# Optimization experiments

Hardware: AMD Instinct MI355X
Metric: run time of the kernel (lower is better)

The kernel has to match this reference:

```python
import jax, jax.numpy as jnp
import numpy as np

V, H_BASE, D, L, K = 32000, 4096, 512, 2, 4
B = 64

def setup_inputs() -> dict:
    key = jax.random.key(0)
    ks = jax.random.split(key, 12)
    s = 0.02
    return {
        "hidden_state": jax.random.normal(ks[0], (B, H_BASE), jnp.float32),
        "in_proj_w": jax.random.normal(ks[1], (D, H_BASE), jnp.float32) * s,
        "in_proj_b": jnp.zeros((D,), jnp.float32),
        "w_ih0": jax.random.normal(ks[2], (3 * D, D), jnp.float32) * s,
        "w_hh0": jax.random.normal(ks[3], (3 * D, D), jnp.float32) * s,
        "b_ih0": jax.random.normal(ks[4], (3 * D,), jnp.float32) * s,
        "b_hh0": jax.random.normal(ks[5], (3 * D,), jnp.float32) * s,
        "w_ih1": jax.random.normal(ks[6], (3 * D, D), jnp.float32) * s,
        "w_hh1": jax.random.normal(ks[7], (3 * D, D), jnp.float32) * s,
        "b_ih1": jax.random.normal(ks[8], (3 * D,), jnp.float32) * s,
        "b_hh1": jax.random.normal(ks[9], (3 * D,), jnp.float32) * s,
        "embed": jax.random.normal(ks[10], (V, D), jnp.float32) * s,
        "out_w": jax.random.normal(ks[11], (V, D), jnp.float32) * s,
    }

def _gru_cell(x, h, w_ih, w_hh, b_ih, b_hh):
    # PyTorch GRU gate order: r, z, n
    gi = x @ w_ih.T + b_ih  # [B, 3D]
    gh = h @ w_hh.T + b_hh
    ir, iz, inn = jnp.split(gi, 3, axis=-1)
    hr, hz, hn = jnp.split(gh, 3, axis=-1)
    r = jax.nn.sigmoid(ir + hr)
    z = jax.nn.sigmoid(iz + hz)
    n = jnp.tanh(inn + r * hn)
    return (1.0 - z) * n + z * h

def reference(hidden_state, in_proj_w, in_proj_b, w_ih0, w_hh0, b_ih0, b_hh0,
              w_ih1, w_hh1, b_ih1, b_hh1, embed, out_w):
    b = hidden_state.shape[0]
    h0 = hidden_state @ in_proj_w.T + in_proj_b  # [B, D]
    h_l0 = h0
    h_l1 = h0
    x = jnp.zeros((b, in_proj_w.shape[0]), hidden_state.dtype)
    all_logits = []
    for _ in range(K):
        h_l0 = _gru_cell(x, h_l0, w_ih0, w_hh0, b_ih0, b_hh0)
        h_l1 = _gru_cell(h_l0, h_l1, w_ih1, w_hh1, b_ih1, b_hh1)
        logits = h_l1 @ out_w.T  # [B, V]
        all_logits.append(logits)
        x = embed[jnp.argmax(logits, axis=-1)]  # greedy next-token embed
    return jnp.stack(all_logits, axis=1)  # [B, K, V]
```

## Files before the change

kernel.cpp:

```cpp
#include <hip/hip_runtime.h>
#include <math.h>


typedef __attribute__((ext_vector_type(8))) short short8;
typedef __attribute__((ext_vector_type(4))) float f32x4;

__device__ __forceinline__ unsigned short f2bf_rne(float x) {
    unsigned u = __float_as_uint(x);
    unsigned r = (u + 0x7fffu + ((u >> 16) & 1u)) >> 16;
    return (unsigned short)r;
}
__device__ __forceinline__ void split2(float x, unsigned short& hi, unsigned short& lo) {
    unsigned u = __float_as_uint(x);
    hi = (unsigned short)(u >> 16);
    float r = x - __uint_as_float(u & 0xffff0000u);
    lo = f2bf_rne(r);
}

__device__ __forceinline__ void store_plane(unsigned short* hiP, unsigned short* loP,
                                            int m, int d, float v) {
    int s = d >> 6, cl = (d >> 3) & 7, e = d & 7;
    int off = m * 512 + s * 64 + ((cl ^ (m & 7)) * 8) + e;
    unsigned short hi, lo; split2(v, hi, lo);
    hiP[off] = hi; loP[off] = lo;
}

__device__ __forceinline__ void gload16(const void* g, void* lds) {
    __builtin_amdgcn_global_load_lds(
        (const __attribute__((address_space(1))) unsigned int*)g,
        (__attribute__((address_space(3))) unsigned int*)lds, 16, 0, 0);
}

__device__ __forceinline__ void split_w_body(
    const float* __restrict__ W, unsigned short* __restrict__ H,
    unsigned short* __restrict__ L, size_t g, int kclog)
{
    int n  = (int)(g >> kclog);
    int c8 = (int)g & ((1 << kclog) - 1);
    const float* src = W + g * 8;
    float4 v0 = *(const float4*)src;
    float4 v1 = *(const float4*)(src + 4);
    unsigned short h[8], l[8];
    split2(v0.x,h[0],l[0]); split2(v0.y,h[1],l[1]); split2(v0.z,h[2],l[2]); split2(v0.w,h[3],l[3]);
    split2(v1.x,h[4],l[4]); split2(v1.y,h[5],l[5]); split2(v1.z,h[6],l[6]); split2(v1.w,h[7],l[7]);
    uint4 ph = make_uint4((unsigned)h[0]|((unsigned)h[1]<<16), (unsigned)h[2]|((unsigned)h[3]<<16),
                          (unsigned)h[4]|((unsigned)h[5]<<16), (unsigned)h[6]|((unsigned)h[7]<<16));
    uint4 pl = make_uint4((unsigned)l[0]|((unsigned)l[1]<<16), (unsigned)l[2]|((unsigned)l[3]<<16),
                          (unsigned)l[4]|((unsigned)l[5]<<16), (unsigned)l[6]|((unsigned)l[7]<<16));
    int nt = n >> 7, row = n & 127;
    int ksi = c8 >> 3;
    int slot = (c8 & 7) ^ (row & 7);
    int tpr = 1 << (kclog - 3);
    size_t off = ((size_t)(nt * tpr + ksi) * 128 + row) * 64 + slot * 8;
    *(uint4*)(H + off) = ph;
    *(uint4*)(L + off) = pl;
}

__global__ __launch_bounds__(256) void k_split_W(
    const float* __restrict__ W, unsigned short* __restrict__ H,
    unsigned short* __restrict__ L, int kclog)
{
    size_t g = (size_t)blockIdx.x * 256 + threadIdx.x;
    split_w_body(W, H, L, g, kclog);
}

__global__ __launch_bounds__(256) void k_split_gw(
    const float* __restrict__ w0, const float* __restrict__ w1,
    const float* __restrict__ w2, const float* __restrict__ w3,
    unsigned short* __restrict__ H, unsigned short* __restrict__ L)
{
    int mat = blockIdx.y;
    const float* W = mat == 0 ? w0 : mat == 1 ? w1 : mat == 2 ? w2 : w3;
    size_t g = (size_t)blockIdx.x * 256 + threadIdx.x;
    split_w_body(W, H + (size_t)mat * 786432, L + (size_t)mat * 786432, g, 6);
}

__global__ __launch_bounds__(256) void k_split_A(
    const float* __restrict__ hidden, char* __restrict__ hidH, char* __restrict__ hidL)
{
    int g = blockIdx.x * 256 + threadIdx.x;
    int m = g >> 9;
    int cc = g & 511;
    int s = cc >> 3, cl = cc & 7;
    const float* src = hidden + m * 4096 + cc * 8;
    float4 v0 = *(const float4*)src;
    float4 v1 = *(const float4*)(src + 4);
    unsigned short h[8], l[8];
    split2(v0.x,h[0],l[0]); split2(v0.y,h[1],l[1]); split2(v0.z,h[2],l[2]); split2(v0.w,h[3],l[3]);
    split2(v1.x,h[4],l[4]); split2(v1.y,h[5],l[5]); split2(v1.z,h[6],l[6]); split2(v1.w,h[7],l[7]);
    uint4 ph = make_uint4((unsigned)h[0]|((unsigned)h[1]<<16), (unsigned)h[2]|((unsigned)h[3]<<16),
                          (unsigned)h[4]|((unsigned)h[5]<<16), (unsigned)h[6]|((unsigned)h[7]<<16));
    uint4 pl = make_uint4((unsigned)l[0]|((unsigned)l[1]<<16), (unsigned)l[2]|((unsigned)l[3]<<16),
                          (unsigned)l[4]|((unsigned)l[5]<<16), (unsigned)l[6]|((unsigned)l[7]<<16));
    int off = m * 8192 + s * 128 + ((cl ^ (m & 7)) * 16);
    *(uint4*)(hidH + off) = ph;
    *(uint4*)(hidL + off) = pl;
}

__device__ __forceinline__ void mfma_core(
    const unsigned short* __restrict__ AsH0, const unsigned short* __restrict__ AsL0,
    const unsigned short* __restrict__ BsH0, const unsigned short* __restrict__ BsL0,
    int wv, int lr, int lh, f32x4* acc)
{
#pragma unroll
    for (int kk2 = 0; kk2 < 2; ++kk2) {
        int aoff = lr * 64 + (((kk2 * 4 + lh) ^ (lr & 7)) * 8);
        short8 ah[4], al[4];
#pragma unroll
        for (int mt = 0; mt < 4; ++mt) {
            ah[mt] = *(const short8*)(AsH0 + mt * 1024 + aoff);
            al[mt] = *(const short8*)(AsL0 + mt * 1024 + aoff);
        }
        int brow = wv * 16 + lr;
        int boff = brow * 64 + (((kk2 * 4 + lh) ^ (brow & 7)) * 8);
        short8 bh = *(const short8*)(BsH0 + boff);
        short8 bl = *(const short8*)(BsL0 + boff);
#pragma unroll
        for (int mt = 0; mt < 4; ++mt) {
            acc[mt] = __builtin_amdgcn_mfma_f32_16x16x32_bf16(ah[mt], bh, acc[mt], 0, 0, 0);
            acc[mt] = __builtin_amdgcn_mfma_f32_16x16x32_bf16(ah[mt], bl, acc[mt], 0, 0, 0);
            acc[mt] = __builtin_amdgcn_mfma_f32_16x16x32_bf16(al[mt], bh, acc[mt], 0, 0, 0);
        }
    }
}

__device__ __forceinline__ void epilogue_write(
    float* __restrict__ C, int ldc, int n0, int wv, int lr, int lh, const f32x4* acc)
{
#pragma unroll
    for (int mt = 0; mt < 4; ++mt)
#pragma unroll
        for (int i = 0; i < 4; ++i) {
            int mm = mt * 16 + lh * 4 + i;
            C[mm * ldc + n0 + wv * 16 + lr] = acc[mt][i];
        }
}

__device__ __forceinline__ void mfma_gemm4(
    const char* __restrict__ AH, const char* __restrict__ AL, int AstrideB, int akk0,
    const unsigned short* __restrict__ BH, const unsigned short* __restrict__ BL,
    size_t btileU, int nk,
    float* __restrict__ C, int ldc, int n0,
    unsigned short (*AsH)[4096], unsigned short (*AsL)[4096],
    unsigned short (*BsH)[4096], unsigned short (*BsL)[4096])
{
    const int tid  = threadIdx.x;
    const int wv   = tid >> 6;
    const int lane = tid & 63;
    const int lr   = lane & 15;
    const int lh   = lane >> 4;
    const int ar1  = wv * 16 + (lane >> 3);
    const int acp  = lane & 7;

    f32x4 acc[4];
#pragma unroll
    for (int i = 0; i < 4; ++i) acc[i] = (f32x4){0.f, 0.f, 0.f, 0.f};

    auto stage = [&](int t, int p) {
        const int kaB = (akk0 + t * 64) * 2;
        gload16(AH + ar1 * AstrideB + kaB + acp * 16,       (char*)AsH[p] + wv * 2048);
        gload16(AH + (ar1 + 8) * AstrideB + kaB + acp * 16, (char*)AsH[p] + wv * 2048 + 1024);
        gload16(AL + ar1 * AstrideB + kaB + acp * 16,       (char*)AsL[p] + wv * 2048);
        gload16(AL + (ar1 + 8) * AstrideB + kaB + acp * 16, (char*)AsL[p] + wv * 2048 + 1024);
        const char* bH = (const char*)BH + (btileU + (size_t)t * 8192) * 2;
        const char* bL = (const char*)BL + (btileU + (size_t)t * 8192) * 2;
        gload16(bH + wv * 2048 +        lane * 16, (char*)BsH[p] + wv * 2048);
        gload16(bH + wv * 2048 + 1024 + lane * 16, (char*)BsH[p] + wv * 2048 + 1024);
        gload16(bL + wv * 2048 +        lane * 16, (char*)BsL[p] + wv * 2048);
        gload16(bL + wv * 2048 + 1024 + lane * 16, (char*)BsL[p] + wv * 2048 + 1024);
    };

    stage(0, 0);
    __syncthreads();

    for (int t = 0; t < nk; ++t) {
        const int p = t & 1;
        if (t + 1 < nk) stage(t + 1, p ^ 1);
        mfma_core(AsH[p], AsL[p], BsH[p], BsL[p], wv, lr, lh, acc);
        __syncthreads();
    }

    epilogue_write(C, ldc, n0, wv, lr, lh, acc);
}

#define DECLARE_LDS4() \
    __shared__ alignas(16) unsigned short AsH[2][4096]; \
    __shared__ alignas(16) unsigned short AsL[2][4096]; \
    __shared__ alignas(16) unsigned short BsH[2][4096]; \
    __shared__ alignas(16) unsigned short BsL[2][4096];

__global__ __launch_bounds__(256) void k_inproj(
    const char* __restrict__ hidH, const char* __restrict__ hidL,
    const unsigned short* __restrict__ WH, const unsigned short* __restrict__ WL,
    float* __restrict__ part)
{
    DECLARE_LDS4();
    int nt2 = blockIdx.x & 7;
    int ks  = blockIdx.x >> 3;
    size_t btile = (size_t)((nt2 >> 1) * 64 + ks * 4) * 8192 + (size_t)(nt2 & 1) * 4096;
    mfma_gemm4(hidH, hidL, 8192, ks * 256,
               WH, WL, btile, 4,
               part + ks * 32768, 512, nt2 * 64,
               AsH, AsL, BsH, BsL);
}

__global__ __launch_bounds__(256) void k_reduce_inproj(
    const float* __restrict__ part, const float* __restrict__ bias,
    float* __restrict__ hA, float* __restrict__ hB,
    unsigned short* hAH, unsigned short* hAL,
    unsigned short* hBH, unsigned short* hBL,
    unsigned short* xH,  unsigned short* xL)
{
    int i = blockIdx.x * 256 + threadIdx.x;
    int b = i >> 9;
    int d = i & 511;
    float s = bias[d];
#pragma unroll
    for (int ks = 0; ks < 16; ++ks) s += part[ks * 32768 + i];
    hA[i] = s;
    hB[i] = s;
    store_plane(hAH, hAL, b, d, s);
    store_plane(hBH, hBL, b, d, s);
    store_plane(xH,  xL,  b, d, 0.f);
}

__global__ __launch_bounds__(256) void k_gates(
    const char* __restrict__ xH, const char* __restrict__ xL,
    const char* __restrict__ hH, const char* __restrict__ hL,
    const unsigned short* __restrict__ gwH, const unsigned short* __restrict__ gwL,
    int layer, float* __restrict__ gip, float* __restrict__ ghp)
{
    DECLARE_LDS4();
    int bx  = blockIdx.x;
    int nt2 = bx % 24;
    int ks  = (bx / 24) & 3;
    int mat = bx / 96;
    const char* AH = mat ? hH : xH;
    const char* AL = mat ? hL : xL;
    float* C = (mat ? ghp : gip) + ks * 98304;
    size_t btile = ((size_t)(layer * 2 + mat) * 96 + (nt2 >> 1) * 8 + ks * 2) * 8192
                 + (size_t)(nt2 & 1) * 4096;
    mfma_gemm4(AH, AL, 1024, ks * 128,
               gwH, gwL, btile, 2,
               C, 1536, nt2 * 64,
               AsH, AsL, BsH, BsL);
}

__global__ __launch_bounds__(256) void k_combine(
    const float* __restrict__ gip, const float* __restrict__ ghp,
    const float* __restrict__ b_ih, const float* __restrict__ b_hh,
    float* __restrict__ h, unsigned short* hH, unsigned short* hL)
{
    int i = blockIdx.x * 256 + threadIdx.x;
    int b = i >> 9;
    int d = i & 511;
    int base = b * 1536 + d;
    float ir = b_ih[d], iz = b_ih[d + 512], inn = b_ih[d + 1024];
    float hr = b_hh[d], hz = b_hh[d + 512], hn = b_hh[d + 1024];
#pragma unroll
    for (int ks = 0; ks < 4; ++ks) {
        const float* gi = gip + ks * 98304 + base;
        const float* gh = ghp + ks * 98304 + base;
        ir  += gi[0];    iz += gi[512];  inn += gi[1024];
        hr  += gh[0];    hz += gh[512];  hn  += gh[1024];
    }
    float r = 1.f / (1.f + expf(-(ir + hr)));
    float z = 1.f / (1.f + expf(-(iz + hz)));
    float n = tanhf(inn + r * hn);
    float hv = (1.f - z) * n + z * h[i];
    h[i] = hv;
    store_plane(hH, hL, b, d, hv);
}

__global__ __launch_bounds__(256) void k_logits(
    const char* __restrict__ hBH, const char* __restrict__ hBL,
    const float* __restrict__ out_w,
    float* __restrict__ out, int step,
    float* __restrict__ pval, int* __restrict__ pidx)
{
    __shared__ alignas(16) unsigned short AsH[2][4096];
    __shared__ alignas(16) unsigned short AsL[2][4096];
    __shared__ alignas(16) unsigned short BsH[2][4096];
    __shared__ alignas(16) unsigned short BsL[2][4096];

    const int tid  = threadIdx.x;
    const int wv   = tid >> 6;
    const int lane = tid & 63;
    const int lr   = lane & 15;
    const int lh   = lane >> 4;
    const int bx   = blockIdx.x;
    const int n0   = bx * 64;

    const int ar1 = wv * 16 + (lane >> 3);
    const int acp = lane & 7;
    auto stageA = [&](int kaB, int p) {
        gload16(hBH + ar1 * 1024 + kaB + acp * 16,       (char*)AsH[p] + wv * 2048);
        gload16(hBH + (ar1 + 8) * 1024 + kaB + acp * 16, (char*)AsH[p] + wv * 2048 + 1024);
        gload16(hBL + ar1 * 1024 + kaB + acp * 16,       (char*)AsL[p] + wv * 2048);
        gload16(hBL + (ar1 + 8) * 1024 + kaB + acp * 16, (char*)AsL[p] + wv * 2048 + 1024);
    };

    const int bn = tid >> 2, bq = tid & 3;
    const float* Wb = out_w + (size_t)(n0 + bn) * 512 + bq * 16;
    const int wo0 = bn * 64 + (((2 * bq)     ^ (bn & 7)) * 8);
    const int wo1 = bn * 64 + (((2 * bq + 1) ^ (bn & 7)) * 8);

    float4 r0, r1, r2, r3;
    auto loadB = [&](int t) {
        const float* s = Wb + t * 64;
        r0 = *(const float4*)s;       r1 = *(const float4*)(s + 4);
        r2 = *(const float4*)(s + 8); r3 = *(const float4*)(s + 12);
    };
    auto writeB = [&](int p) {
        unsigned short h[16], l[16];
        split2(r0.x,h[0],l[0]);   split2(r0.y,h[1],l[1]);   split2(r0.z,h[2],l[2]);   split2(r0.w,h[3],l[3]);
        split2(r1.x,h[4],l[4]);   split2(r1.y,h[5],l[5]);   split2(r1.z,h[6],l[6]);   split2(r1.w,h[7],l[7]);
        split2(r2.x,h[8],l[8]);   split2(r2.y,h[9],l[9]);   split2(r2.z,h[10],l[10]); split2(r2.w,h[11],l[11]);
        split2(r3.x,h[12],l[12]); split2(r3.y,h[13],l[13]); split2(r3.z,h[14],l[14]); split2(r3.w,h[15],l[15]);
        *(uint4*)(BsH[p] + wo0) = make_uint4(
            (unsigned)h[0]|((unsigned)h[1]<<16),  (unsigned)h[2]|((unsigned)h[3]<<16),
            (unsigned)h[4]|((unsigned)h[5]<<16),  (unsigned)h[6]|((unsigned)h[7]<<16));
        *(uint4*)(BsH[p] + wo1) = make_uint4(
            (unsigned)h[8]|((unsigned)h[9]<<16),  (unsigned)h[10]|((unsigned)h[11]<<16),
            (unsigned)h[12]|((unsigned)h[13]<<16),(unsigned)h[14]|((unsigned)h[15]<<16));
        *(uint4*)(BsL[p] + wo0) = make_uint4(
            (unsigned)l[0]|((unsigned)l[1]<<16),  (unsigned)l[2]|((unsigned)l[3]<<16),
            (unsigned)l[4]|((unsigned)l[5]<<16),  (unsigned)l[6]|((unsigned)l[7]<<16));
        *(uint4*)(BsL[p] + wo1) = make_uint4(
            (unsigned)l[8]|((unsigned)l[9]<<16),  (unsigned)l[10]|((unsigned)l[11]<<16),
            (unsigned)l[12]|((unsigned)l[13]<<16),(unsigned)l[14]|((unsigned)l[15]<<16));
    };

    f32x4 acc[4];
#pragma unroll
    for (int i = 0; i < 4; ++i) acc[i] = (f32x4){0.f, 0.f, 0.f, 0.f};

    loadB(0);
    stageA(0, 0);
    writeB(0);
    __syncthreads();
#pragma unroll
    for (int t = 0; t < 8; ++t) {
        const int p = t & 1;
        if (t < 7) { loadB(t + 1); stageA((t + 1) * 128, p ^ 1); }
        mfma_core(AsH[p], AsL[p], BsH[p], BsL[p], wv, lr, lh, acc);
        if (t < 7) writeB(p ^ 1);
        __syncthreads();
    }

    epilogue_write(out + step * 32000, 128000, n0, wv, lr, lh, acc);

    float* sv = (float*)&AsH[0][0];
    int*   sc = (int*)&AsL[0][0];
#pragma unroll
    for (int mt = 0; mt < 4; ++mt)
#pragma unroll
        for (int i = 0; i < 4; ++i) {
            float v = acc[mt][i];
            int   c = n0 + wv * 16 + lr;
#pragma unroll
            for (int msk = 1; msk < 16; msk <<= 1) {
                float ov = __shfl_xor(v, msk, 64);
                int   oc = __shfl_xor(c, msk, 64);
                if (ov > v || (ov == v && oc < c)) { v = ov; c = oc; }
            }
            if (lr == 0) {
                int row = mt * 16 + lh * 4 + i;
                sv[wv * 64 + row] = v;
                sc[wv * 64 + row] = c;
            }
        }
    __syncthreads();
    if (tid < 64) {
        float v = sv[tid]; int c = sc[tid];
#pragma unroll
        for (int w = 1; w < 4; ++w) {
            float ov = sv[w * 64 + tid]; int oc = sc[w * 64 + tid];
            if (ov > v || (ov == v && oc < c)) { v = ov; c = oc; }
        }
        pval[bx * 64 + tid] = v;
        pidx[bx * 64 + tid] = c;
    }
}

__global__ __launch_bounds__(256) void k_reduce_embed(
    const float* __restrict__ pval, const int* __restrict__ pidx,
    const float* __restrict__ embed, unsigned short* xH, unsigned short* xL)
{
    __shared__ float sv[256];
    __shared__ int   sc[256];
    const int b = blockIdx.x;
    const int tid = threadIdx.x;
    float v = pval[tid * 64 + b];
    int   c = pidx[tid * 64 + b];
    if (tid + 256 < 500) {
        float ov = pval[(tid + 256) * 64 + b];
        int   oc = pidx[(tid + 256) * 64 + b];
        if (ov > v || (ov == v && oc < c)) { v = ov; c = oc; }
    }
    sv[tid] = v; sc[tid] = c;
    __syncthreads();
    for (int s = 128; s > 0; s >>= 1) {
        if (tid < s) {
            float ov = sv[tid + s]; int oc = sc[tid + s];
            if (ov > sv[tid] || (ov == sv[tid] && oc < sc[tid])) { sv[tid] = ov; sc[tid] = oc; }
        }
        __syncthreads();
    }
    int tok = sc[0];
    for (int j = tid; j < 512; j += 256)
        store_plane(xH, xL, b, j, embed[(size_t)tok * 512 + j]);
}

extern "C" void kernel_launch(void* const* d_in, const int* in_sizes, int n_in,
                              void* d_out, int out_size, void* d_ws, size_t ws_size,
                              hipStream_t stream)
{
    const float* hidden = (const float*)d_in[0];
    const float* in_w   = (const float*)d_in[1];
    const float* in_b   = (const float*)d_in[2];
    const float* w_ih0  = (const float*)d_in[3];
    const float* w_hh0  = (const float*)d_in[4];
    const float* b_ih0  = (const float*)d_in[5];
    const float* b_hh0  = (const float*)d_in[6];
    const float* w_ih1  = (const float*)d_in[7];
    const float* w_hh1  = (const float*)d_in[8];
    const float* b_ih1  = (const float*)d_in[9];
    const float* b_hh1  = (const float*)d_in[10];
    const float* embed  = (const float*)d_in[11];
    const float* out_w  = (const float*)d_in[12];
    float* out = (float*)d_out;
    char*  ws  = (char*)d_ws;

    float* hA  = (float*)(ws + 0);
    float* hB  = (float*)(ws + 131072);
    unsigned short* xH  = (unsigned short*)(ws + 262144);
    unsigned short* xL  = (unsigned short*)(ws + 327680);
    unsigned short* hAH = (unsigned short*)(ws + 393216);
    unsigned short* hAL = (unsigned short*)(ws + 458752);
    unsigned short* hBH = (unsigned short*)(ws + 524288);
    unsigned short* hBL = (unsigned short*)(ws + 589824);
    char* hidH = ws + 655360;
    char* hidL = ws + 1179648;
    float* gip = (float*)(ws + 1703936);
    float* ghp = (float*)(ws + 3276800);
    float* pval = (float*)(ws + 4849664);
    int*   pidx = (int*)  (ws + 4980736);
    float* ipart = (float*)(ws + 5111808);
    unsigned short* gwH = (unsigned short*)(ws + 7208960);
    unsigned short* gwL = (unsigned short*)(ws + 13500416);
    unsigned short* inH = (unsigned short*)(ws + 19791872);
    unsigned short* inL = (unsigned short*)(ws + 23986176);

    k_split_A<<<128, 256, 0, stream>>>(hidden, hidH, hidL);
    k_split_gw<<<dim3(384, 4), 256, 0, stream>>>(w_ih0, w_hh0, w_ih1, w_hh1, gwH, gwL);
    k_split_W<<<1024, 256, 0, stream>>>(in_w, inH, inL, 9);
    k_inproj<<<128, 256, 0, stream>>>(hidH, hidL, inH, inL, ipart);
    k_reduce_inproj<<<128, 256, 0, stream>>>(ipart, in_b, hA, hB,
                                             hAH, hAL, hBH, hBL, xH, xL);

    for (int step = 0; step < 4; ++step) {
        k_gates<<<192, 256, 0, stream>>>((char*)xH, (char*)xL, (char*)hAH, (char*)hAL,
                                         gwH, gwL, 0, gip, ghp);
        k_combine<<<128, 256, 0, stream>>>(gip, ghp, b_ih0, b_hh0, hA, hAH, hAL);
        k_gates<<<192, 256, 0, stream>>>((char*)hAH, (char*)hAL, (char*)hBH, (char*)hBL,
                                         gwH, gwL, 1, gip, ghp);
        k_combine<<<128, 256, 0, stream>>>(gip, ghp, b_ih1, b_hh1, hB, hBH, hBL);
        k_logits<<<500, 256, 0, stream>>>((char*)hBH, (char*)hBL, out_w,
                                          out, step, pval, pidx);
        k_reduce_embed<<<64, 256, 0, stream>>>(pval, pidx, embed, xH, xL);
    }
}
```

Measured before the change: 353.2 us.

## Fuse argmax reduction and embedding gather into layer-0 gate GEMM

Removes the separate argmax-reduce/embed kernel. Each layer-0 input-gate block now redoes the final argmax over transposed partial results and splits the gathered embedding rows into its own LDS A tile. At step 0 it just writes zeros, since x is zero. This saves one launch per step and the round trip of x through global memory, at the cost of every one of the 96 input-gate blocks repeating the 64x500 argmax reduction.

```diff
diff --git a/kernel.cpp b/kernel.cpp
--- a/kernel.cpp
+++ b/kernel.cpp
@@ -208,8 +208,7 @@
     const float* __restrict__ part, const float* __restrict__ bias,
     float* __restrict__ hA, float* __restrict__ hB,
     unsigned short* hAH, unsigned short* hAL,
-    unsigned short* hBH, unsigned short* hBL,
-    unsigned short* xH,  unsigned short* xL)
+    unsigned short* hBH, unsigned short* hBL)
 {
     int i = blockIdx.x * 256 + threadIdx.x;
     int b = i >> 9;
@@ -221,7 +220,104 @@
     hB[i] = s;
     store_plane(hAH, hAL, b, d, s);
     store_plane(hBH, hBL, b, d, s);
-    store_plane(xH,  xL,  b, d, 0.f);
+}
+
+__global__ __launch_bounds__(256) void k_gates_l0(
+    int step,
+    const float* __restrict__ pvT, const int* __restrict__ piT,
+    const float* __restrict__ embed,
+    const char* __restrict__ hAH, const char* __restrict__ hAL,
+    const unsigned short* __restrict__ gwH, const unsigned short* __restrict__ gwL,
+    float* __restrict__ gip, float* __restrict__ ghp)
+{
+    DECLARE_LDS4();
+    __shared__ int stok[64];
+    const int bx = blockIdx.x, tid = threadIdx.x;
+    const int nt2 = bx % 24, ks = (bx / 24) & 3, mat = bx / 96;
+
+    if (mat) {
+        size_t btile = ((size_t)96 + (nt2 >> 1) * 8 + ks * 2) * 8192
+                     + (size_t)(nt2 & 1) * 4096;
+        mfma_gemm4(hAH, hAL, 1024, ks * 128, gwH, gwL, btile, 2,
+                   ghp + ks * 98304, 1536, nt2 * 64, AsH, AsL, BsH, BsL);
+        return;
+    }
+
+    float* C = gip + ks * 98304;
+    if (step == 0) {
+        float4 z = make_float4(0.f, 0.f, 0.f, 0.f);
+        for (int q = tid; q < 1024; q += 256) {
+            int r2 = q >> 4, cq = q & 15;
+            *(float4*)(C + r2 * 1536 + nt2 * 64 + cq * 4) = z;
+        }
+        return;
+    }
+
+    const int wv = tid >> 6, lane = tid & 63, lr = lane & 15, lh = lane >> 4;
+    const size_t btileU = ((size_t)((nt2 >> 1) * 8 + ks * 2)) * 8192
+                        + (size_t)(nt2 & 1) * 4096;
+    auto stageB = [&](int t, int p) {
+        const char* bH = (const char*)gwH + (btileU + (size_t)t * 8192) * 2;
+        const char* bL = (const char*)gwL + (btileU + (size_t)t * 8192) * 2;
+        gload16(bH + wv * 2048 +        lane * 16, (char*)BsH[p] + wv * 2048);
+        gload16(bH + wv * 2048 + 1024 + lane * 16, (char*)BsH[p] + wv * 2048 + 1024);
+        gload16(bL + wv * 2048 +        lane * 16, (char*)BsL[p] + wv * 2048);
+        gload16(bL + wv * 2048 + 1024 + lane * 16, (char*)BsL[p] + wv * 2048 + 1024);
+    };
+
+    stageB(0, 0);
+
+    {
+        int r = tid >> 2, j0 = tid & 3;
+        float v = -3.4e38f; int c = 0x7fffffff;
+        for (int j = j0; j < 500; j += 4) {
+            float ov = pvT[r * 512 + j]; int oc = piT[r * 512 + j];
+            if (ov > v || (ov == v && oc < c)) { v = ov; c = oc; }
+        }
+#pragma unroll
+        for (int msk = 1; msk < 4; msk <<= 1) {
+            float ov = __shfl_xor(v, msk, 64);
+            int   oc = __shfl_xor(c, msk, 64);
+            if (ov > v || (ov == v && oc < c)) { v = ov; c = oc; }
+        }
+        if (j0 == 0) stok[r] = c;
+    }
+    __syncthreads();
+
+    {
+        int mm = tid >> 2, cl0 = (tid & 3) * 2;
+        int tok = stok[mm];
+        int obase = (mm >> 4) * 1024 + (mm & 15) * 64;
+#pragma unroll
+        for (int t2 = 0; t2 < 2; ++t2) {
+#pragma unroll
+            for (int u = 0; u < 2; ++u) {
+                int cl = cl0 + u;
+                const float* src = embed + (size_t)tok * 512 + ks * 128 + t2 * 64 + cl * 8;
+                float4 v0 = *(const float4*)src;
+                float4 v1 = *(const float4*)(src + 4);
+                unsigned short h[8], l[8];
+                split2(v0.x,h[0],l[0]); split2(v0.y,h[1],l[1]); split2(v0.z,h[2],l[2]); split2(v0.w,h[3],l[3]);
+                split2(v1.x,h[4],l[4]); split2(v1.y,h[5],l[5]); split2(v1.z,h[6],l[6]); split2(v1.w,h[7],l[7]);
+                uint4 ph = make_uint4((unsigned)h[0]|((unsigned)h[1]<<16), (unsigned)h[2]|((unsigned)h[3]<<16),
+                                      (unsigned)h[4]|((unsigned)h[5]<<16), (unsigned)h[6]|((unsigned)h[7]<<16));
+                uint4 pl = make_uint4((unsigned)l[0]|((unsigned)l[1]<<16), (unsigned)l[2]|((unsigned)l[3]<<16),
+                                      (unsigned)l[4]|((unsigned)l[5]<<16), (unsigned)l[6]|((unsigned)l[7]<<16));
+                int off = obase + ((cl ^ (mm & 7)) * 8);
+                *(uint4*)(AsH[t2] + off) = ph;
+                *(uint4*)(AsL[t2] + off) = pl;
+            }
+        }
+    }
+    stageB(1, 1);
+    __syncthreads();
+
+    f32x4 acc[4];
+#pragma unroll
+    for (int i = 0; i < 4; ++i) acc[i] = (f32x4){0.f, 0.f, 0.f, 0.f};
+    mfma_core(AsH[0], AsL[0], BsH[0], BsL[0], wv, lr, lh, acc);
+    mfma_core(AsH[1], AsL[1], BsH[1], BsL[1], wv, lr, lh, acc);
+    epilogue_write(C, 1536, nt2 * 64, wv, lr, lh, acc);
 }
 
 __global__ __launch_bounds__(256) void k_gates(
@@ -276,7 +372,7 @@
     const char* __restrict__ hBH, const char* __restrict__ hBL,
     const float* __restrict__ out_w,
     float* __restrict__ out, int step,
-    float* __restrict__ pval, int* __restrict__ pidx)
+    float* __restrict__ pvT, int* __restrict__ piT)
 {
     __shared__ alignas(16) unsigned short AsH[2][4096];
     __shared__ alignas(16) unsigned short AsL[2][4096];
@@ -378,38 +474,9 @@
             float ov = sv[w * 64 + tid]; int oc = sc[w * 64 + tid];
             if (ov > v || (ov == v && oc < c)) { v = ov; c = oc; }
         }
-        pval[bx * 64 + tid] = v;
-        pidx[bx * 64 + tid] = c;
-    }
-}
-
-__global__ __launch_bounds__(256) void k_reduce_embed(
-    const float* __restrict__ pval, const int* __restrict__ pidx,
-    const float* __restrict__ embed, unsigned short* xH, unsigned short* xL)
-{
-    __shared__ float sv[256];
-    __shared__ int   sc[256];
-    const int b = blockIdx.x;
-    const int tid = threadIdx.x;
-    float v = pval[tid * 64 + b];
-    int   c = pidx[tid * 64 + b];
-    if (tid + 256 < 500) {
-        float ov = pval[(tid + 256) * 64 + b];
-        int   oc = pidx[(tid + 256) * 64 + b];
-        if (ov > v || (ov == v && oc < c)) { v = ov; c = oc; }
-    }
-    sv[tid] = v; sc[tid] = c;
-    __syncthreads();
-    for (int s = 128; s > 0; s >>= 1) {
-        if (tid < s) {
-            float ov = sv[tid + s]; int oc = sc[tid + s];
-            if (ov > sv[tid] || (ov == sv[tid] && oc < sc[tid])) { sv[tid] = ov; sc[tid] = oc; }
-        }
-        __syncthreads();
-    }
-    int tok = sc[0];
-    for (int j = tid; j < 512; j += 256)
-        store_plane(xH, xL, b, j, embed[(size_t)tok * 512 + j]);
+        pvT[tid * 512 + bx] = v;
+        piT[tid * 512 + bx] = c;
+    }
 }
 
 extern "C" void kernel_launch(void* const* d_in, const int* in_sizes, int n_in,
@@ -434,8 +501,6 @@
 
     float* hA  = (float*)(ws + 0);
     float* hB  = (float*)(ws + 131072);
-    unsigned short* xH  = (unsigned short*)(ws + 262144);
-    unsigned short* xL  = (unsigned short*)(ws + 327680);
     unsigned short* hAH = (unsigned short*)(ws + 393216);
     unsigned short* hAL = (unsigned short*)(ws + 458752);
     unsigned short* hBH = (unsigned short*)(ws + 524288);
@@ -444,8 +509,8 @@
     char* hidL = ws + 1179648;
     float* gip = (float*)(ws + 1703936);
     float* ghp = (float*)(ws + 3276800);
-    float* pval = (float*)(ws + 4849664);
-    int*   pidx = (int*)  (ws + 4980736);
+    float* pvT = (float*)(ws + 4849664);
+    int*   piT = (int*)  (ws + 4980736);
     float* ipart = (float*)(ws + 5111808);
     unsigned short* gwH = (unsigned short*)(ws + 7208960);
     unsigned short* gwL = (unsigned short*)(ws + 13500416);
@@ -457,17 +522,17 @@
     k_split_W<<<1024, 256, 0, stream>>>(in_w, inH, inL, 9);
     k_inproj<<<128, 256, 0, stream>>>(hidH, hidL, inH, inL, ipart);
     k_reduce_inproj<<<128, 256, 0, stream>>>(ipart, in_b, hA, hB,
-                                             hAH, hAL, hBH, hBL, xH, xL);
+                                             hAH, hAL, hBH, hBL);
 
     for (int step = 0; step < 4; ++step) {
-        k_gates<<<192, 256, 0, stream>>>((char*)xH, (char*)xL, (char*)hAH, (char*)hAL,
-                                         gwH, gwL, 0, gip, ghp);
+        k_gates_l0<<<192, 256, 0, stream>>>(step, pvT, piT, embed,
+                                            (char*)hAH, (char*)hAL,
+                                            gwH, gwL, gip, ghp);
         k_combine<<<128, 256, 0, stream>>>(gip, ghp, b_ih0, b_hh0, hA, hAH, hAL);
         k_gates<<<192, 256, 0, stream>>>((char*)hAH, (char*)hAL, (char*)hBH, (char*)hBL,
                                          gwH, gwL, 1, gip, ghp);
         k_combine<<<128, 256, 0, stream>>>(gip, ghp, b_ih1, b_hh1, hB, hBH, hBL);
         k_logits<<<500, 256, 0, stream>>>((char*)hBH, (char*)hBL, out_w,
-                                          out, step, pval, pidx);
-        k_reduce_embed<<<64, 256, 0, stream>>>(pval, pidx, embed, xH, xL);
-    }
-}
+                                          out, step, pvT, piT);
+    }
+}
```

After: 392.2 us. 1.11x slower.
